# Kernel optimization log

Hardware: AMD Instinct MI355X
Metric: run time of the kernel (lower is better)

Reference implementation:

```python
import jax, jax.numpy as jnp
import numpy as np

B, NP, NR = 4, 2048, 10
EDGE_F = 32
EMB = 64          # emb_features == out_features (required for layer stacking)
ESM_EMB = 64
HEADS = 16
NUM_LAYERS = 4
LN_EPS = 1e-5


def _ln(x, g, b):
    mu = jnp.mean(x, axis=-1, keepdims=True)
    var = jnp.var(x, axis=-1, keepdims=True)
    return (x - mu) / jnp.sqrt(var + LN_EPS) * g + b


def setup_inputs() -> dict:
    key = jax.random.key(0)
    ks = jax.random.split(key, 32)
    s = 0.05  # xavier-ish scale for weights
    inp = {
        "pep_feat": jax.random.normal(ks[0], (B, NP, 27 + 1280), jnp.float32),
        "rec_feat": jax.random.normal(ks[1], (B, NP, NR, 42 + 1280), jnp.float32),
        "edge_feat": jax.random.normal(ks[2], (B, NP, NR, EDGE_F), jnp.float32),
        # embedding weights (torch Linear convention: y = x @ W.T)
        "W_rec_esm": jax.random.normal(ks[3], (ESM_EMB, 1280), jnp.float32) * s,
        "W_pep_esm": jax.random.normal(ks[4], (ESM_EMB, 1280), jnp.float32) * s,
        "W_pep_emb": jax.random.normal(ks[5], (EMB, 27 + ESM_EMB), jnp.float32) * s,
        "W_rec_emb": jax.random.normal(ks[6], (EMB, 21 + ESM_EMB), jnp.float32) * s,
        "W_edge_emb": jax.random.normal(ks[7], (EMB, EDGE_F), jnp.float32) * s,
        "pep_ln_g": jnp.ones((EMB,), jnp.float32),
        "pep_ln_b": jnp.zeros((EMB,), jnp.float32),
        "rec_ln_g": jnp.ones((EMB,), jnp.float32),
        "rec_ln_b": jnp.zeros((EMB,), jnp.float32),
        # stacked GraphAttention layer params [L, ...]
        "ga_Wp": jax.random.normal(ks[8], (NUM_LAYERS, EMB, EMB), jnp.float32) * s,
        "ga_bp": jnp.zeros((NUM_LAYERS, EMB), jnp.float32),
        "ga_Wr": jax.random.normal(ks[9], (NUM_LAYERS, EMB, 2 * EMB), jnp.float32) * s,
        "ga_br": jnp.zeros((NUM_LAYERS, EMB), jnp.float32),
        "ga_Wv": jax.random.normal(ks[10], (NUM_LAYERS, EMB, 2 * EMB), jnp.float32) * s,
        "ga_bv": jnp.zeros((NUM_LAYERS, EMB), jnp.float32),
        # self-attention pooling: LN + MLP [64 -> 64 -> 32 -> 16 heads], no biases
        "pool_ln_g": jnp.ones((EMB,), jnp.float32),
        "pool_ln_b": jnp.zeros((EMB,), jnp.float32),
        "pool_W0": jax.random.normal(ks[11], (EMB, EMB), jnp.float32) * s,
        "pool_W1": jax.random.normal(ks[12], (EMB // 2, EMB), jnp.float32) * s,
        "pool_W2": jax.random.normal(ks[13], (HEADS, EMB // 2), jnp.float32) * s,
        # final projection
        "mlp_W": jax.random.normal(ks[14], (EMB // 2, EMB), jnp.float32) * s,
        "mlp_b": jnp.zeros((EMB // 2,), jnp.float32),
    }
    return inp


def _forward(pep_feat, rec_feat, edge_feat, W_rec_esm, W_pep_esm, W_pep_emb,
             W_rec_emb, W_edge_emb, pep_ln_g, pep_ln_b, rec_ln_g, rec_ln_b,
             ga_Wp, ga_bp, ga_Wr, ga_br, ga_Wv, ga_bv,
             pool_ln_g, pool_ln_b, pool_W0, pool_W1, pool_W2, mlp_W, mlp_b):
    # --- embeddings ---
    rec_esm = rec_feat[..., 42:] @ W_rec_esm.T                       # [B,NP,10,ESM]
    pep_esm = pep_feat[..., -1280:] @ W_pep_esm.T                    # [B,NP,ESM]
    rec = jnp.concatenate([rec_feat[..., :21], rec_esm], axis=-1) @ W_rec_emb.T
    pep = jnp.concatenate([pep_feat[..., :27], pep_esm], axis=-1) @ W_pep_emb.T
    edge = edge_feat @ W_edge_emb.T                                  # [B,NP,10,EMB]
    pep = _ln(pep, pep_ln_g, pep_ln_b)
    rec = _ln(rec, rec_ln_g, rec_ln_b)

    inv_sqrt_d = 1.0 / np.sqrt(EMB).astype(np.float32)
    rec_edge = jnp.concatenate([rec, edge], axis=-1)                 # [B,NP,10,2*EMB]
    # --- stacked GraphAttention layers (dropout = eval-mode identity) ---
    for l in range(NUM_LAYERS):
        q = pep @ ga_Wp[l].T + ga_bp[l]                              # [B,NP,EMB]
        key = rec_edge @ ga_Wr[l].T + ga_br[l]                       # [B,NP,10,EMB]
        val = rec_edge @ ga_Wv[l].T + ga_bv[l]                       # [B,NP,10,EMB]
        logit = jnp.einsum('bpd,bprd->bpr', q, key) * inv_sqrt_d     # [B,NP,10]
        attn = jax.nn.softmax(logit, axis=-1)
        pep = q + jnp.einsum('bpr,bprd->bpd', attn, val)             # [B,NP,EMB]

    # --- self-attention pooling (note: softmax applied twice, as in source) ---
    d = _ln(pep, pool_ln_g, pool_ln_b)                               # [B,NP,EMB]
    h = jnp.tanh(d @ pool_W0.T)
    h = jnp.tanh(h @ pool_W1.T)
    logits = h @ pool_W2.T                                           # [B,NP,HEADS]
    a = jax.nn.softmax(logits, axis=1)
    a = jax.nn.softmax(a, axis=1)
    attended = jnp.einsum('bsh,bsd->bhd', a, d)                      # [B,HEADS,EMB]
    pooled = attended.mean(axis=1)                                   # [B,EMB]
    return pooled @ mlp_W.T + mlp_b                                  # [B,EMB//2]


def reference(pep_feat, rec_feat, edge_feat, W_rec_esm, W_pep_esm, W_pep_emb,
              W_rec_emb, W_edge_emb, pep_ln_g, pep_ln_b, rec_ln_g, rec_ln_b,
              ga_Wp, ga_bp, ga_Wr, ga_br, ga_Wv, ga_bv,
              pool_ln_g, pool_ln_b, pool_W0, pool_W1, pool_W2, mlp_W, mlp_b):
    return _forward(pep_feat, rec_feat, edge_feat, W_rec_esm, W_pep_esm, W_pep_emb,
                    W_rec_emb, W_edge_emb, pep_ln_g, pep_ln_b, rec_ln_g, rec_ln_b,
                    ga_Wp, ga_bp, ga_Wr, ga_br, ga_Wv, ga_bv,
                    pool_ln_g, pool_ln_b, pool_W0, pool_W1, pool_W2, mlp_W, mlp_b)
```

## Files before the change

kernel.cpp:

```cpp
#include <hip/hip_runtime.h>
#include <hip/hip_bf16.h>


typedef __attribute__((ext_vector_type(8))) short bf16x8;
typedef __attribute__((ext_vector_type(4))) float f32x4;

#define MFMA(a, b, c) __builtin_amdgcn_mfma_f32_16x16x32_bf16((a), (b), (c), 0, 0, 0)

#define WB_REC_OFF   0
#define WB_PEP_OFF   83968
#define WB_EDGE_OFF  167936
#define WB_P_OFF     169984
#define WB_R_OFF     186368
#define WB_V_OFF     219136
#define WB_W0_OFF    251904
#define WB_W1_OFF    256000
#define WB_W2_OFF    258048
#define WB_TOTAL     258560

__device__ __forceinline__ unsigned short f2bf(float x) {
  __hip_bfloat16 h = __float2bfloat16(x);
  return __builtin_bit_cast(unsigned short, h);
}
__device__ __forceinline__ float bf2f(unsigned short u) {
  unsigned int t = ((unsigned int)u) << 16;
  return __builtin_bit_cast(float, t);
}
__device__ __forceinline__ bf16x8 loadBc(const unsigned short* base, int chunk, int lane) {
  return *(const bf16x8*)(base + ((size_t)chunk * 64 + lane) * 8);
}
__device__ __forceinline__ float tanhf_fast(float x) {
  float e = __expf(2.f * x);
  return 1.f - 2.f / (e + 1.f);
}
__device__ __forceinline__ int swzr(int r) {
  return (r & 1) | (((r >> 1) & 7) << 2);
}

__global__ __launch_bounds__(256) void k_pack(
    const float* __restrict__ Wresm, const float* __restrict__ Wpesm,
    const float* __restrict__ Wre, const float* __restrict__ Wpe,
    const float* __restrict__ Wedge, const float* __restrict__ Wp,
    const float* __restrict__ Wr, const float* __restrict__ Wv,
    const float* __restrict__ W0, const float* __restrict__ W1,
    const float* __restrict__ W2, unsigned short* __restrict__ WB) {
  const int t = blockIdx.x * 256 + threadIdx.x;
  if (t >= WB_TOTAL) return;
  float v = 0.f;
  if (t < WB_EDGE_OFF) {
    bool isPep = (t >= WB_PEP_OFF);
    int u = isPep ? (t - WB_PEP_OFF) : t;
    int j = u & 7, lane = (u >> 3) & 63, n = (u >> 9) & 3, kc = u >> 11;
    int k = kc * 32 + ((lane >> 4) << 3) + j;
    int col = n * 16 + (lane & 15);
    if (kc < 40) {
      const float* wemb = isPep ? (Wpe + col * 91 + 27) : (Wre + col * 85 + 21);
      const float* wesm = isPep ? Wpesm : Wresm;
      float s = 0.f;
#pragma unroll 8
      for (int e = 0; e < 64; ++e) s += wemb[e] * wesm[e * 1280 + k];
      v = s;
    } else {
      int kl = k - 1280;
      if (isPep) v = (kl < 27) ? Wpe[col * 91 + kl] : 0.f;
      else       v = (kl < 21) ? Wre[col * 85 + kl] : 0.f;
    }
  } else if (t < WB_P_OFF) {
    int u = t - WB_EDGE_OFF;
    int j = u & 7, lane = (u >> 3) & 63, n = (u >> 9) & 3;
    v = Wedge[(n * 16 + (lane & 15)) * 32 + ((lane >> 4) << 3) + j];
  } else if (t < WB_R_OFF) {
    int u = t - WB_P_OFF;
    int l = u >> 12, w = u & 4095;
    int j = w & 7, lane = (w >> 3) & 63, n = (w >> 9) & 3, kc = w >> 11;
    int o = kc * 32 + ((lane >> 4) << 3) + j;
    int d = n * 16 + (lane & 15);
    v = Wp[l * 4096 + d * 64 + o];
  } else if (t < WB_V_OFF) {
    int u = t - WB_R_OFF;
    int l = u >> 13, w = u & 8191;
    int j = w & 7, lane = (w >> 3) & 63, c = (w >> 9) & 15;
    int kc = c >> 3, n = c & 7;
    int o = kc * 32 + ((lane >> 4) << 3) + j;
    int k = n * 16 + (lane & 15);
    v = Wr[l * 8192 + o * 128 + k];
  } else if (t < WB_W0_OFF) {
    int u = t - WB_V_OFF;
    int l = u >> 13, w = u & 8191;
    int j = w & 7, lane = (w >> 3) & 63, n = (w >> 9) & 3, kc = w >> 11;
    int k = kc * 32 + ((lane >> 4) << 3) + j;
    int d = n * 16 + (lane & 15);
    v = Wv[l * 8192 + d * 128 + k];
  } else if (t < WB_W1_OFF) {
    int u = t - WB_W0_OFF;
    int j = u & 7, lane = (u >> 3) & 63, c = u >> 9;
    int kc = c >> 2, n = c & 3;
    v = W0[(n * 16 + (lane & 15)) * 64 + kc * 32 + ((lane >> 4) << 3) + j];
  } else if (t < WB_W2_OFF) {
    int u = t - WB_W1_OFF;
    int j = u & 7, lane = (u >> 3) & 63, c = u >> 9;
    int kc = c >> 1, n = c & 1;
    v = W1[(n * 16 + (lane & 15)) * 64 + kc * 32 + ((lane >> 4) << 3) + j];
  } else {
    int u = t - WB_W2_OFF;
    int j = u & 7, lane = (u >> 3) & 63;
    v = W2[(lane & 15) * 32 + ((lane >> 4) << 3) + j];
  }
  WB[t] = f2bf(v);
}

__global__ __launch_bounds__(64) void k_emb(
    const float* __restrict__ rec_feat, const float* __restrict__ edge_feat,
    const float* __restrict__ pep_feat, const unsigned short* __restrict__ WB,
    const float* __restrict__ rec_g, const float* __restrict__ rec_b,
    const float* __restrict__ pep_g, const float* __restrict__ pep_b,
    unsigned short* __restrict__ rec_edge, unsigned short* __restrict__ pep_out) {
  __shared__ float stg[2][16][128];
  const int bid = blockIdx.x;
  const int lane = threadIdx.x;
  const int quad = lane >> 4, lr = lane & 15;
  const bool isPep = (bid >= 5120);
  const int brow = (isPep ? bid - 5120 : bid) * 16;

  const f32x4 fz = {0.f, 0.f, 0.f, 0.f};
  f32x4 acc[4] = {fz, fz, fz, fz};

  auto frag = [&](int buf, int c) -> bf16x8 {
    const int u0 = c * 8 + quad * 2;
    const int s0 = u0 ^ swzr(lr), s1 = (u0 + 1) ^ swzr(lr);
    const float4 f0 = *(const float4*)((const char*)&stg[buf][lr][0] + s0 * 16);
    const float4 f1 = *(const float4*)((const char*)&stg[buf][lr][0] + s1 * 16);
    bf16x8 a;
#pragma unroll
    for (int j = 0; j < 4; ++j) { a[j] = (short)f2bf(f0[j]); a[4 + j] = (short)f2bf(f1[j]); }
    return a;
  };

  if (!isPep) {
    const float* base = rec_feat + (size_t)brow * 1322 + 42;
    float2 ld2[16];
    auto loadg = [&](int g) {
#pragma unroll
      for (int i = 0; i < 16; ++i)
        ld2[i] = *(const float2*)(base + (size_t)i * 1322 + g * 128 + lane * 2);
    };
    auto writeg = [&](int b) {
#pragma unroll
      for (int i = 0; i < 16; ++i) {
        const int su = (lane >> 1) ^ swzr(i);
        *(float2*)((char*)&stg[b][i][0] + su * 16 + (lane & 1) * 8) = ld2[i];
      }
    };
    loadg(0); writeg(0);
    int buf = 0;
    for (int g = 0; g < 10; ++g) {
      bf16x8 bb[16];
#pragma unroll
      for (int m = 0; m < 16; ++m) bb[m] = loadBc(WB + WB_REC_OFF, g * 16 + m, lane);
      if (g < 9) loadg(g + 1);
#pragma unroll
      for (int c = 0; c < 4; ++c) {
        const bf16x8 a = frag(buf, c);
#pragma unroll
        for (int n = 0; n < 4; ++n) acc[n] = MFMA(a, bb[c * 4 + n], acc[n]);
      }
      if (g < 9) writeg(buf ^ 1);
      buf ^= 1;
    }
    {
      const float* p = rec_feat + (size_t)(brow + lr) * 1322 + quad * 8;
      bf16x8 a;
#pragma unroll
      for (int m = 0; m < 4; ++m) {
        const float2 v = *(const float2*)(p + 2 * m);
        a[2 * m] = (short)f2bf(v.x); a[2 * m + 1] = (short)f2bf(v.y);
      }
#pragma unroll
      for (int n = 0; n < 4; ++n)
        acc[n] = MFMA(a, loadBc(WB + WB_REC_OFF, 160 + n, lane), acc[n]);
    }
  } else {
    const float* base = pep_feat + (size_t)brow * 1307 + 27;
    float ldp[32];
    auto loadg = [&](int g) {
#pragma unroll
      for (int i = 0; i < 16; ++i)
#pragma unroll
        for (int ph = 0; ph < 2; ++ph)
          ldp[i * 2 + ph] = base[(size_t)i * 1307 + g * 128 + ph * 64 + lane];
    };
    auto writeg = [&](int b) {
#pragma unroll
      for (int i = 0; i < 16; ++i)
#pragma unroll
        for (int ph = 0; ph < 2; ++ph) {
          const int su = (ph * 16 + (lane >> 2)) ^ swzr(i);
          *((float*)((char*)&stg[b][i][0] + su * 16 + (lane & 3) * 4)) = ldp[i * 2 + ph];
        }
    };
    loadg(0); writeg(0);
    int buf = 0;
    for (int g = 0; g < 10; ++g) {
      bf16x8 bb[16];
#pragma unroll
      for (int m = 0; m < 16; ++m) bb[m] = loadBc(WB + WB_PEP_OFF, g * 16 + m, lane);
      if (g < 9) loadg(g + 1);
#pragma unroll
      for (int c = 0; c < 4; ++c) {
        const bf16x8 a = frag(buf, c);
#pragma unroll
        for (int n = 0; n < 4; ++n) acc[n] = MFMA(a, bb[c * 4 + n], acc[n]);
      }
      if (g < 9) writeg(buf ^ 1);
      buf ^= 1;
    }
    {
      const float* p = pep_feat + (size_t)(brow + lr) * 1307 + quad * 8;
      bf16x8 a;
#pragma unroll
      for (int j = 0; j < 8; ++j) a[j] = (short)f2bf(p[j]);
#pragma unroll
      for (int n = 0; n < 4; ++n)
        acc[n] = MFMA(a, loadBc(WB + WB_PEP_OFF, 160 + n, lane), acc[n]);
    }
  }

  float s[4], sq[4];
#pragma unroll
  for (int i = 0; i < 4; ++i) {
    s[i] = acc[0][i] + acc[1][i] + acc[2][i] + acc[3][i];
    sq[i] = acc[0][i] * acc[0][i] + acc[1][i] * acc[1][i] +
            acc[2][i] * acc[2][i] + acc[3][i] * acc[3][i];
  }
#pragma unroll
  for (int msk = 1; msk < 16; msk <<= 1) {
#pragma unroll
    for (int i = 0; i < 4; ++i) {
      s[i] += __shfl_xor(s[i], msk);
      sq[i] += __shfl_xor(sq[i], msk);
    }
  }
  const float* gp = isPep ? pep_g : rec_g;
  const float* bp = isPep ? pep_b : rec_b;
  float gv[4], bvl[4];
#pragma unroll
  for (int n = 0; n < 4; ++n) { gv[n] = gp[lr + 16 * n]; bvl[n] = bp[lr + 16 * n]; }

  if (!isPep) {
    f32x4 acce[4] = {fz, fz, fz, fz};
    {
      const float* p = edge_feat + (size_t)(brow + lr) * 32 + quad * 8;
      const float4 f0 = *(const float4*)(p);
      const float4 f1 = *(const float4*)(p + 4);
      bf16x8 a;
#pragma unroll
      for (int j = 0; j < 4; ++j) { a[j] = (short)f2bf(f0[j]); a[4 + j] = (short)f2bf(f1[j]); }
#pragma unroll
      for (int n = 0; n < 4; ++n) acce[n] = MFMA(a, loadBc(WB + WB_EDGE_OFF, n, lane), acce[n]);
    }
#pragma unroll
    for (int i = 0; i < 4; ++i) {
      const float mean = s[i] * (1.f / 64.f);
      const float var = sq[i] * (1.f / 64.f) - mean * mean;
      const float rstd = rsqrtf(var + 1e-5f);
      unsigned short* dst = rec_edge + (size_t)(brow + quad * 4 + i) * 128;
#pragma unroll
      for (int n = 0; n < 4; ++n) {
        dst[lr + 16 * n] = f2bf((acc[n][i] - mean) * rstd * gv[n] + bvl[n]);
        dst[64 + lr + 16 * n] = f2bf(acce[n][i]);
      }
    }
  } else {
#pragma unroll
    for (int i = 0; i < 4; ++i) {
      const float mean = s[i] * (1.f / 64.f);
      const float var = sq[i] * (1.f / 64.f) - mean * mean;
      const float rstd = rsqrtf(var + 1e-5f);
      unsigned short* dst = pep_out + (size_t)(brow + quad * 4 + i) * 64;
#pragma unroll
      for (int n = 0; n < 4; ++n)
        dst[lr + 16 * n] = f2bf((acc[n][i] - mean) * rstd * gv[n] + bvl[n]);
    }
  }
}

__global__ __launch_bounds__(256) void k_ga(
    const unsigned short* __restrict__ rec_edge, const unsigned short* __restrict__ pep_bf,
    const unsigned short* __restrict__ WB,
    const float* __restrict__ ga_bp, const float* __restrict__ ga_bv,
    const float* __restrict__ pool_g, const float* __restrict__ pool_b,
    float* __restrict__ dbuf, float* __restrict__ logitsT) {
  __shared__ unsigned short pep_s[1024];
  __shared__ unsigned short q_s[1024];
  __shared__ __align__(16) unsigned short zs[2048];
  __shared__ float bias_s[512];
  __shared__ float lgp[4][10][17];
  __shared__ float redp[4][2][16];
  __shared__ float oap[4][16][68];

  const int tid = threadIdx.x;
  const int w = tid >> 6;
  const int lane = tid & 63;
  const int quad = lane >> 4, lr = lane & 15;
  const int swz = lr & 7;
  const int pbase = blockIdx.x * 16;
  const int mycol = lr + 16 * w;
  const f32x4 fz = {0.f, 0.f, 0.f, 0.f};

  bias_s[tid] = ga_bp[tid & 255];
  bias_s[256 + tid] = ga_bv[tid & 255];
  if (tid < 128) {
    const int p = tid >> 3, gg = tid & 7;
    const bf16x8 v = *(const bf16x8*)(pep_bf + (size_t)(pbase + p) * 64 + gg * 8);
    *(bf16x8*)(pep_s + p * 64 + ((gg ^ (p & 7)) << 3)) = v;
  }
  const unsigned short* reb =
      rec_edge + (size_t)(pbase + lr) * 1280 + w * 32 + quad * 8;
  bf16x8 rfs[10];
#pragma unroll
  for (int r = 0; r < 10; ++r) rfs[r] = *(const bf16x8*)(reb + r * 128);
  __syncthreads();

  auto bwrite = [&](unsigned short* buf, int p, int col, unsigned short val) {
    buf[p * 64 + ((((col >> 3)) ^ (p & 7)) << 3) + (col & 7)] = val;
  };
  auto bfrag = [&](const unsigned short* buf, int kc) -> bf16x8 {
    return *(const bf16x8*)(buf + lr * 64 + ((((kc << 2) + quad) ^ swz) << 3));
  };

  f32x4 pcur;
  for (int l = 0; l < 4; ++l) {
    const unsigned short* WBp = WB + WB_P_OFF + l * 4096;
    const unsigned short* WBr = WB + WB_R_OFF + l * 8192;
    const unsigned short* WBv = WB + WB_V_OFF + l * 8192;

    f32x4 qa = fz;
    qa = MFMA(bfrag(pep_s, 0), loadBc(WBp, w, lane), qa);
    qa = MFMA(bfrag(pep_s, 1), loadBc(WBp, 4 + w, lane), qa);
    const float bpv = bias_s[l * 64 + mycol];
#pragma unroll
    for (int i = 0; i < 4; ++i) qa[i] += bpv;
#pragma unroll
    for (int i = 0; i < 4; ++i) bwrite(q_s, quad * 4 + i, mycol, f2bf(qa[i]));
    __syncthreads();

    const bf16x8 aq0 = bfrag(q_s, 0), aq1 = bfrag(q_s, 1);
    f32x4 za0 = fz, za1 = fz;
    za0 = MFMA(aq0, loadBc(WBr, 2 * w, lane), za0);
    za0 = MFMA(aq1, loadBc(WBr, 8 + 2 * w, lane), za0);
    za1 = MFMA(aq0, loadBc(WBr, 2 * w + 1, lane), za1);
    za1 = MFMA(aq1, loadBc(WBr, 9 + 2 * w, lane), za1);
#pragma unroll
    for (int i = 0; i < 4; ++i) {
      const int p = quad * 4 + i;
      const int k0 = 16 * (2 * w) + lr, k1 = 16 * (2 * w + 1) + lr;
      zs[p * 128 + ((((k0 >> 3) ^ (p & 7)) << 3) | (k0 & 7))] = f2bf(za0[i]);
      zs[p * 128 + ((((k1 >> 3) ^ (p & 7)) << 3) | (k1 & 7))] = f2bf(za1[i]);
    }
    float zfw[8];
    {
      const bf16x8 z8 = *(const bf16x8*)(zs + lr * 128 + (((quad + 4 * w) ^ swz) << 3));
#pragma unroll
      for (int j = 0; j < 8; ++j) zfw[j] = bf2f((unsigned short)z8[j]);
    }
#pragma unroll
    for (int r = 0; r < 10; ++r) {
      float part = 0.f;
#pragma unroll
      for (int j = 0; j < 8; ++j) part += bf2f((unsigned short)rfs[r][j]) * zfw[j];
      part += __shfl_xor(part, 16);
      part += __shfl_xor(part, 32);
      if (quad == 0) lgp[w][r][lr] = part;
    }
    __syncthreads();
    float lg[10];
#pragma unroll
    for (int r = 0; r < 10; ++r)
      lg[r] = (lgp[0][r][lr] + lgp[1][r][lr] + lgp[2][r][lr] + lgp[3][r][lr]) * 0.125f;
    float mx = lg[0];
#pragma unroll
    for (int r = 1; r < 10; ++r) mx = fmaxf(mx, lg[r]);
    float ssum = 0.f;
#pragma unroll
    for (int r = 0; r < 10; ++r) { lg[r] = __expf(lg[r] - mx); ssum += lg[r]; }
    const float inv = 1.f / ssum;
#pragma unroll
    for (int r = 0; r < 10; ++r) lg[r] *= inv;
    float wsacc[8] = {};
#pragma unroll
    for (int r = 0; r < 10; ++r)
#pragma unroll
      for (int j = 0; j < 8; ++j)
        wsacc[j] += lg[r] * bf2f((unsigned short)rfs[r][j]);
    bf16x8 wf;
#pragma unroll
    for (int j = 0; j < 8; ++j) wf[j] = (short)f2bf(wsacc[j]);
    f32x4 oa[4];
#pragma unroll
    for (int n = 0; n < 4; ++n) oa[n] = MFMA(wf, loadBc(WBv, w * 4 + n, lane), fz);
#pragma unroll
    for (int n = 0; n < 4; ++n)
#pragma unroll
      for (int i = 0; i < 4; ++i)
        oap[w][quad * 4 + i][n * 16 + lr] = oa[n][i];
    __syncthreads();
    const float bvv = bias_s[256 + l * 64 + mycol];
#pragma unroll
    for (int i = 0; i < 4; ++i) {
      const int p = quad * 4 + i;
      const float o = oap[0][p][mycol] + oap[1][p][mycol] +
                      oap[2][p][mycol] + oap[3][p][mycol];
      pcur[i] = qa[i] + o + bvv;
    }
#pragma unroll
    for (int i = 0; i < 4; ++i) bwrite(pep_s, quad * 4 + i, mycol, f2bf(pcur[i]));
    __syncthreads();
  }

  {
    float s[4], sq[4];
#pragma unroll
    for (int i = 0; i < 4; ++i) { s[i] = pcur[i]; sq[i] = pcur[i] * pcur[i]; }
#pragma unroll
    for (int msk = 1; msk < 16; msk <<= 1) {
#pragma unroll
      for (int i = 0; i < 4; ++i) {
        s[i] += __shfl_xor(s[i], msk);
        sq[i] += __shfl_xor(sq[i], msk);
      }
    }
    if (lr == 0) {
#pragma unroll
      for (int i = 0; i < 4; ++i) {
        redp[w][0][quad * 4 + i] = s[i];
        redp[w][1][quad * 4 + i] = sq[i];
      }
    }
    __syncthreads();
    const float gv = pool_g[mycol], bv2 = pool_b[mycol];
    float d[4];
    float* zf32 = (float*)zs;
#pragma unroll
    for (int i = 0; i < 4; ++i) {
      const int p = quad * 4 + i;
      const float sf = redp[0][0][p] + redp[1][0][p] + redp[2][0][p] + redp[3][0][p];
      const float sqf = redp[0][1][p] + redp[1][1][p] + redp[2][1][p] + redp[3][1][p];
      const float mean = sf * (1.f / 64.f);
      const float var = sqf * (1.f / 64.f) - mean * mean;
      const float rstd = rsqrtf(var + 1e-5f);
      d[i] = (pcur[i] - mean) * rstd * gv + bv2;
      zf32[p * 64 + mycol] = d[i];
      bwrite(q_s, p, mycol, f2bf(d[i]));
    }
    __syncthreads();
    {
      const float4 v = *(const float4*)(&zf32[tid * 4]);
      *(float4*)(dbuf + (size_t)pbase * 64 + tid * 4) = v;
    }
    if (w == 0) {
      const bf16x8 ad0 = bfrag(q_s, 0), ad1 = bfrag(q_s, 1);
      f32x4 h0[4] = {fz, fz, fz, fz};
#pragma unroll
      for (int n = 0; n < 4; ++n) {
        h0[n] = MFMA(ad0, loadBc(WB + WB_W0_OFF, n, lane), h0[n]);
        h0[n] = MFMA(ad1, loadBc(WB + WB_W0_OFF, 4 + n, lane), h0[n]);
      }
#pragma unroll
      for (int n = 0; n < 4; ++n)
#pragma unroll
        for (int i = 0; i < 4; ++i)
          bwrite(q_s, quad * 4 + i, lr + 16 * n, f2bf(tanhf_fast(h0[n][i])));
      const bf16x8 ah00 = bfrag(q_s, 0), ah01 = bfrag(q_s, 1);
      f32x4 h1[2] = {fz, fz};
#pragma unroll
      for (int n = 0; n < 2; ++n) {
        h1[n] = MFMA(ah00, loadBc(WB + WB_W1_OFF, n, lane), h1[n]);
        h1[n] = MFMA(ah01, loadBc(WB + WB_W1_OFF, 2 + n, lane), h1[n]);
      }
#pragma unroll
      for (int n = 0; n < 2; ++n)
#pragma unroll
        for (int i = 0; i < 4; ++i)
          bwrite(q_s, quad * 4 + i, lr + 16 * n, f2bf(tanhf_fast(h1[n][i])));
      const bf16x8 ah1 = bfrag(q_s, 0);
      f32x4 lac = MFMA(ah1, loadBc(WB + WB_W2_OFF, 0, lane), fz);
      const int b = pbase >> 11, sx0 = pbase & 2047;
#pragma unroll
      for (int i = 0; i < 4; ++i)
        logitsT[(size_t)(b * 16 + lr) * 2048 + sx0 + quad * 4 + i] = lac[i];
    }
  }
}

__global__ __launch_bounds__(256) void k_pool2(
    const float* __restrict__ logitsT, const float* __restrict__ dbuf,
    float* __restrict__ attp) {
  __shared__ float sh[2048];
  __shared__ float red[8];
  __shared__ float part[16][64];
  const int blk = blockIdx.x;
  const int bh = blk >> 2, q = blk & 3;
  const int b = bh >> 4;
  const int tid = threadIdx.x, lane = tid & 63, wid = tid >> 6;
  const float* lrow = logitsT + (size_t)bh * 2048;

  float m = -1e30f;
  for (int sx = tid; sx < 2048; sx += 256) {
    float v = lrow[sx];
    sh[sx] = v;
    m = fmaxf(m, v);
  }
#pragma unroll
  for (int msk = 1; msk < 64; msk <<= 1) m = fmaxf(m, __shfl_xor(m, msk));
  if (lane == 0) red[wid] = m;
  __syncthreads();
  m = fmaxf(fmaxf(red[0], red[1]), fmaxf(red[2], red[3]));

  float s1 = 0.f;
  for (int sx = tid; sx < 2048; sx += 256) {
    float e = __expf(sh[sx] - m);
    sh[sx] = e;
    s1 += e;
  }
#pragma unroll
  for (int msk = 1; msk < 64; msk <<= 1) s1 += __shfl_xor(s1, msk);
  __syncthreads();
  if (lane == 0) red[4 + wid] = s1;
  __syncthreads();
  s1 = red[4] + red[5] + red[6] + red[7];
  const float invS1 = 1.f / s1;

  float s2 = 0.f;
  for (int sx = tid; sx < 2048; sx += 256) {
    float e2 = __expf((sh[sx] - 1.f) * invS1);
    sh[sx] = e2;
    s2 += e2;
  }
#pragma unroll
  for (int msk = 1; msk < 64; msk <<= 1) s2 += __shfl_xor(s2, msk);
  __syncthreads();
  if (lane == 0) red[wid] = s2;
  __syncthreads();
  s2 = red[0] + red[1] + red[2] + red[3];
  const float invS2 = 1.f / s2;

  const int d16 = tid & 15, sxg = tid >> 4;
  float4 a4 = {0.f, 0.f, 0.f, 0.f};
  const float* db = dbuf + (size_t)b * 2048 * 64 + d16 * 4;
#pragma unroll 4
  for (int sx = q * 512 + sxg; sx < (q + 1) * 512; sx += 16) {
    const float w = sh[sx];
    const float4 v = *(const float4*)(db + (size_t)sx * 64);
    a4.x += w * v.x; a4.y += w * v.y; a4.z += w * v.z; a4.w += w * v.w;
  }
  *(float4*)(&part[sxg][d16 * 4]) = a4;
  __syncthreads();
  if (tid < 64) {
    float s = 0.f;
#pragma unroll
    for (int g2 = 0; g2 < 16; ++g2) s += part[g2][tid];
    attp[(size_t)(bh * 4 + q) * 64 + tid] = s * invS2;
  }
}

__global__ __launch_bounds__(256) void k_final(
    const float* __restrict__ attp, const float* __restrict__ W,
    const float* __restrict__ bias, float* __restrict__ out) {
  __shared__ float pooled[4][64];
  const int tid = threadIdx.x;
  {
    const int b = tid >> 6, d = tid & 63;
    float s = 0.f;
#pragma unroll
    for (int hq = 0; hq < 64; ++hq) s += attp[((size_t)b * 64 + hq) * 64 + d];
    pooled[b][d] = s * (1.f / 16.f);
  }
  __syncthreads();
  if (tid < 128) {
    const int b = tid >> 5, j = tid & 31;
    float s = bias[j];
#pragma unroll
    for (int d2 = 0; d2 < 64; ++d2) s += pooled[b][d2] * W[j * 64 + d2];
    out[b * 32 + j] = s;
  }
}

extern "C" void kernel_launch(void* const* d_in, const int* in_sizes, int n_in,
                              void* d_out, int out_size, void* d_ws, size_t ws_size,
                              hipStream_t stream) {
  const float* pep_feat = (const float*)d_in[0];
  const float* rec_feat = (const float*)d_in[1];
  const float* edge_feat = (const float*)d_in[2];
  const float* W_rec_esm = (const float*)d_in[3];
  const float* W_pep_esm = (const float*)d_in[4];
  const float* W_pep_emb = (const float*)d_in[5];
  const float* W_rec_emb = (const float*)d_in[6];
  const float* W_edge_emb = (const float*)d_in[7];
  const float* pep_ln_g = (const float*)d_in[8];
  const float* pep_ln_b = (const float*)d_in[9];
  const float* rec_ln_g = (const float*)d_in[10];
  const float* rec_ln_b = (const float*)d_in[11];
  const float* ga_Wp = (const float*)d_in[12];
  const float* ga_bp = (const float*)d_in[13];
  const float* ga_Wr = (const float*)d_in[14];
  const float* ga_br = (const float*)d_in[15];
  const float* ga_Wv = (const float*)d_in[16];
  const float* ga_bv = (const float*)d_in[17];
  const float* pool_ln_g = (const float*)d_in[18];
  const float* pool_ln_b = (const float*)d_in[19];
  const float* pool_W0 = (const float*)d_in[20];
  const float* pool_W1 = (const float*)d_in[21];
  const float* pool_W2 = (const float*)d_in[22];
  const float* mlp_W = (const float*)d_in[23];
  const float* mlp_b = (const float*)d_in[24];
  float* out = (float*)d_out;
  (void)ga_br;
  (void)ws_size; (void)in_sizes; (void)n_in; (void)out_size;

  char* ws = (char*)d_ws;
  unsigned short* WB = (unsigned short*)(ws);
  unsigned short* rec_edge = (unsigned short*)(ws + 524288);
  unsigned short* pep_bf = (unsigned short*)(ws + 21495808);
  float* dbuf = (float*)(ws + 22544384);
  float* logitsT = (float*)(ws + 24641536);
  float* attp = (float*)(ws + 25165824);

  k_pack<<<1010, 256, 0, stream>>>(W_rec_esm, W_pep_esm, W_rec_emb, W_pep_emb,
                                   W_edge_emb, ga_Wp, ga_Wr, ga_Wv,
                                   pool_W0, pool_W1, pool_W2, WB);
  k_emb<<<5632, 64, 0, stream>>>(rec_feat, edge_feat, pep_feat, WB,
                                 rec_ln_g, rec_ln_b, pep_ln_g, pep_ln_b,
                                 rec_edge, pep_bf);
  k_ga<<<512, 256, 0, stream>>>(rec_edge, pep_bf, WB, ga_bp, ga_bv,
                                pool_ln_g, pool_ln_b, dbuf, logitsT);
  k_pool2<<<256, 256, 0, stream>>>(logitsT, dbuf, attp);
  k_final<<<1, 256, 0, stream>>>(attp, mlp_W, mlp_b, out);
}
```

Measured before the change: 170.3 us.

## Process two row tiles per embedding block with aligned vector loads and shifted weight packing

The embedding kernel now handles 32 rows per block instead of 16, so each loaded B fragment feeds two MFMA tiles and weight traffic per row is halved. The feature columns are re-based to 16-byte-aligned offsets (40 for rec, 24 for pep), so rows can be read with dwordx4/dwordx2 inline-asm loads. To keep the maths unchanged, the packed weights are shifted and the boundary columns are moved into the tail chunk. Explicit vmcnt waits replace compiler-tracked dependencies. This raises register and LDS use per block, halves the grid, and adds fragile index remapping.

Measured after the change: 181.9 us. +6.8%, slower.

```diff
diff --git a/kernel.cpp b/kernel.cpp
--- a/kernel.cpp
+++ b/kernel.cpp
@@ -4,6 +4,7 @@
 
 typedef __attribute__((ext_vector_type(8))) short bf16x8;
 typedef __attribute__((ext_vector_type(4))) float f32x4;
+typedef __attribute__((ext_vector_type(2))) float f32x2;
 
 #define MFMA(a, b, c) __builtin_amdgcn_mfma_f32_16x16x32_bf16((a), (b), (c), 0, 0, 0)
 
@@ -53,17 +54,31 @@
     int j = u & 7, lane = (u >> 3) & 63, n = (u >> 9) & 3, kc = u >> 11;
     int k = kc * 32 + ((lane >> 4) << 3) + j;
     int col = n * 16 + (lane & 15);
-    if (kc < 40) {
-      const float* wemb = isPep ? (Wpe + col * 91 + 27) : (Wre + col * 85 + 21);
-      const float* wesm = isPep ? Wpesm : Wresm;
+    const float* wemb = isPep ? (Wpe + col * 91 + 27) : (Wre + col * 85 + 21);
+    const float* wesm = isPep ? Wpesm : Wresm;
+    auto comb = [&](int e_idx) {
       float s = 0.f;
 #pragma unroll 8
-      for (int e = 0; e < 64; ++e) s += wemb[e] * wesm[e * 1280 + k];
-      v = s;
+      for (int e = 0; e < 64; ++e) s += wemb[e] * wesm[e * 1280 + e_idx];
+      return s;
+    };
+    if (kc < 40) {
+      if (!isPep) {
+        v = (k >= 2) ? comb(k - 2) : 0.f;
+      } else {
+        v = (k < 3) ? Wpe[col * 91 + 24 + k] : comb(k - 3);
+      }
     } else {
       int kl = k - 1280;
-      if (isPep) v = (kl < 27) ? Wpe[col * 91 + kl] : 0.f;
-      else       v = (kl < 21) ? Wre[col * 85 + kl] : 0.f;
+      if (!isPep) {
+        if (kl <= 20) v = Wre[col * 85 + kl];
+        else if (kl <= 22) v = comb(1278 + (kl - 21));
+        else v = 0.f;
+      } else {
+        if (kl <= 23) v = Wpe[col * 91 + kl];
+        else if (kl <= 26) v = comb(1277 + (kl - 24));
+        else v = 0.f;
+      }
     }
   } else if (t < WB_P_OFF) {
     int u = t - WB_EDGE_OFF;
@@ -115,21 +130,26 @@
     const float* __restrict__ rec_g, const float* __restrict__ rec_b,
     const float* __restrict__ pep_g, const float* __restrict__ pep_b,
     unsigned short* __restrict__ rec_edge, unsigned short* __restrict__ pep_out) {
-  __shared__ float stg[2][16][128];
+  __shared__ float stg[2][2][16][128];
   const int bid = blockIdx.x;
   const int lane = threadIdx.x;
   const int quad = lane >> 4, lr = lane & 15;
-  const bool isPep = (bid >= 5120);
-  const int brow = (isPep ? bid - 5120 : bid) * 16;
+  const bool isPep = (bid >= 2560);
+  const int brow = (isPep ? bid - 2560 : bid) * 32;
+  const unsigned short* WBb = WB + (isPep ? WB_PEP_OFF : WB_REC_OFF);
 
   const f32x4 fz = {0.f, 0.f, 0.f, 0.f};
-  f32x4 acc[4] = {fz, fz, fz, fz};
-
-  auto frag = [&](int buf, int c) -> bf16x8 {
+  f32x4 acc[2][4];
+#pragma unroll
+  for (int tt = 0; tt < 2; ++tt)
+#pragma unroll
+    for (int n = 0; n < 4; ++n) acc[tt][n] = fz;
+
+  auto frag = [&](int b, int tt, int c) -> bf16x8 {
     const int u0 = c * 8 + quad * 2;
     const int s0 = u0 ^ swzr(lr), s1 = (u0 + 1) ^ swzr(lr);
-    const float4 f0 = *(const float4*)((const char*)&stg[buf][lr][0] + s0 * 16);
-    const float4 f1 = *(const float4*)((const char*)&stg[buf][lr][0] + s1 * 16);
+    const float4 f0 = *(const float4*)((const char*)&stg[b][tt][lr][0] + s0 * 16);
+    const float4 f1 = *(const float4*)((const char*)&stg[b][tt][lr][0] + s1 * 16);
     bf16x8 a;
 #pragma unroll
     for (int j = 0; j < 4; ++j) { a[j] = (short)f2bf(f0[j]); a[4 + j] = (short)f2bf(f1[j]); }
@@ -137,149 +157,183 @@
   };
 
   if (!isPep) {
-    const float* base = rec_feat + (size_t)brow * 1322 + 42;
-    float2 ld2[16];
+    f32x4 a4[16];
     auto loadg = [&](int g) {
 #pragma unroll
-      for (int i = 0; i < 16; ++i)
-        ld2[i] = *(const float2*)(base + (size_t)i * 1322 + g * 128 + lane * 2);
+      for (int ii = 0; ii < 16; ++ii) {
+        const int rr = 2 * ii + (lane >> 5);
+        const float* p = rec_feat + (size_t)(brow + rr) * 1322 + 40 + g * 128 + (lane & 31) * 4;
+        asm volatile("global_load_dwordx4 %0, %1, off" : "=v"(a4[ii]) : "v"(p));
+      }
     };
     auto writeg = [&](int b) {
 #pragma unroll
-      for (int i = 0; i < 16; ++i) {
-        const int su = (lane >> 1) ^ swzr(i);
-        *(float2*)((char*)&stg[b][i][0] + su * 16 + (lane & 1) * 8) = ld2[i];
+      for (int ii = 0; ii < 16; ++ii) {
+        const int rr = 2 * ii + (lane >> 5);
+        const int tt = rr >> 4, ri = rr & 15;
+        const int su = (lane & 31) ^ swzr(ri);
+        *(f32x4*)((char*)&stg[b][tt][ri][0] + su * 16) = a4[ii];
       }
     };
-    loadg(0); writeg(0);
+    loadg(0);
+    asm volatile("s_waitcnt vmcnt(0)" ::: "memory");
+    writeg(0);
     int buf = 0;
     for (int g = 0; g < 10; ++g) {
-      bf16x8 bb[16];
-#pragma unroll
-      for (int m = 0; m < 16; ++m) bb[m] = loadBc(WB + WB_REC_OFF, g * 16 + m, lane);
       if (g < 9) loadg(g + 1);
 #pragma unroll
       for (int c = 0; c < 4; ++c) {
-        const bf16x8 a = frag(buf, c);
-#pragma unroll
-        for (int n = 0; n < 4; ++n) acc[n] = MFMA(a, bb[c * 4 + n], acc[n]);
-      }
-      if (g < 9) writeg(buf ^ 1);
+        bf16x8 bb[4];
+#pragma unroll
+        for (int n = 0; n < 4; ++n) bb[n] = loadBc(WBb, g * 16 + c * 4 + n, lane);
+        const bf16x8 a0 = frag(buf, 0, c), a1 = frag(buf, 1, c);
+#pragma unroll
+        for (int n = 0; n < 4; ++n) {
+          acc[0][n] = MFMA(a0, bb[n], acc[0][n]);
+          acc[1][n] = MFMA(a1, bb[n], acc[1][n]);
+        }
+      }
+      if (g < 9) {
+        asm volatile("s_waitcnt vmcnt(0)" ::: "memory");
+        writeg(buf ^ 1);
+      }
       buf ^= 1;
     }
-    {
-      const float* p = rec_feat + (size_t)(brow + lr) * 1322 + quad * 8;
+#pragma unroll
+    for (int tt = 0; tt < 2; ++tt) {
+      const float* row = rec_feat + (size_t)(brow + 16 * tt + lr) * 1322;
       bf16x8 a;
 #pragma unroll
-      for (int m = 0; m < 4; ++m) {
-        const float2 v = *(const float2*)(p + 2 * m);
-        a[2 * m] = (short)f2bf(v.x); a[2 * m + 1] = (short)f2bf(v.y);
+      for (int j = 0; j < 8; ++j) {
+        const int pos = quad * 8 + j;
+        float x = 0.f;
+        if (pos <= 20) x = row[pos];
+        else if (pos == 21) x = row[1320];
+        else if (pos == 22) x = row[1321];
+        a[j] = (short)f2bf(x);
       }
 #pragma unroll
       for (int n = 0; n < 4; ++n)
-        acc[n] = MFMA(a, loadBc(WB + WB_REC_OFF, 160 + n, lane), acc[n]);
+        acc[tt][n] = MFMA(a, loadBc(WBb, 160 + n, lane), acc[tt][n]);
     }
   } else {
-    const float* base = pep_feat + (size_t)brow * 1307 + 27;
-    float ldp[32];
+    f32x2 a2[32];
     auto loadg = [&](int g) {
 #pragma unroll
-      for (int i = 0; i < 16; ++i)
-#pragma unroll
-        for (int ph = 0; ph < 2; ++ph)
-          ldp[i * 2 + ph] = base[(size_t)i * 1307 + g * 128 + ph * 64 + lane];
+      for (int i = 0; i < 32; ++i) {
+        const float* p = pep_feat + (size_t)(brow + i) * 1307 + 24 + g * 128 + lane * 2;
+        asm volatile("global_load_dwordx2 %0, %1, off" : "=v"(a2[i]) : "v"(p));
+      }
     };
     auto writeg = [&](int b) {
 #pragma unroll
-      for (int i = 0; i < 16; ++i)
-#pragma unroll
-        for (int ph = 0; ph < 2; ++ph) {
-          const int su = (ph * 16 + (lane >> 2)) ^ swzr(i);
-          *((float*)((char*)&stg[b][i][0] + su * 16 + (lane & 3) * 4)) = ldp[i * 2 + ph];
-        }
+      for (int i = 0; i < 32; ++i) {
+        const int tt = i >> 4, ri = i & 15;
+        const int su = (lane >> 1) ^ swzr(ri);
+        *(f32x2*)((char*)&stg[b][tt][ri][0] + su * 16 + (lane & 1) * 8) = a2[i];
+      }
     };
-    loadg(0); writeg(0);
+    loadg(0);
+    asm volatile("s_waitcnt vmcnt(0)" ::: "memory");
+    writeg(0);
     int buf = 0;
     for (int g = 0; g < 10; ++g) {
-      bf16x8 bb[16];
-#pragma unroll
-      for (int m = 0; m < 16; ++m) bb[m] = loadBc(WB + WB_PEP_OFF, g * 16 + m, lane);
       if (g < 9) loadg(g + 1);
 #pragma unroll
       for (int c = 0; c < 4; ++c) {
-        const bf16x8 a = frag(buf, c);
-#pragma unroll
-        for (int n = 0; n < 4; ++n) acc[n] = MFMA(a, bb[c * 4 + n], acc[n]);
-      }
-      if (g < 9) writeg(buf ^ 1);
+        bf16x8 bb[4];
+#pragma unroll
+        for (int n = 0; n < 4; ++n) bb[n] = loadBc(WBb, g * 16 + c * 4 + n, lane);
+        const bf16x8 a0 = frag(buf, 0, c), a1 = frag(buf, 1, c);
+#pragma unroll
+        for (int n = 0; n < 4; ++n) {
+          acc[0][n] = MFMA(a0, bb[n], acc[0][n]);
+          acc[1][n] = MFMA(a1, bb[n], acc[1][n]);
+        }
+      }
+      if (g < 9) {
+        asm volatile("s_waitcnt vmcnt(0)" ::: "memory");
+        writeg(buf ^ 1);
+      }
       buf ^= 1;
     }
-    {
-      const float* p = pep_feat + (size_t)(brow + lr) * 1307 + quad * 8;
+#pragma unroll
+    for (int tt = 0; tt < 2; ++tt) {
+      const float* row = pep_feat + (size_t)(brow + 16 * tt + lr) * 1307;
       bf16x8 a;
 #pragma unroll
-      for (int j = 0; j < 8; ++j) a[j] = (short)f2bf(p[j]);
+      for (int j = 0; j < 8; ++j) {
+        const int pos = quad * 8 + j;
+        float x = 0.f;
+        if (pos <= 23) x = row[pos];
+        else if (pos <= 26) x = row[1304 + (pos - 24)];
+        a[j] = (short)f2bf(x);
+      }
 #pragma unroll
       for (int n = 0; n < 4; ++n)
-        acc[n] = MFMA(a, loadBc(WB + WB_PEP_OFF, 160 + n, lane), acc[n]);
-    }
-  }
-
-  float s[4], sq[4];
-#pragma unroll
-  for (int i = 0; i < 4; ++i) {
-    s[i] = acc[0][i] + acc[1][i] + acc[2][i] + acc[3][i];
-    sq[i] = acc[0][i] * acc[0][i] + acc[1][i] * acc[1][i] +
-            acc[2][i] * acc[2][i] + acc[3][i] * acc[3][i];
-  }
-#pragma unroll
-  for (int msk = 1; msk < 16; msk <<= 1) {
-#pragma unroll
-    for (int i = 0; i < 4; ++i) {
-      s[i] += __shfl_xor(s[i], msk);
-      sq[i] += __shfl_xor(sq[i], msk);
-    }
-  }
+        acc[tt][n] = MFMA(a, loadBc(WBb, 160 + n, lane), acc[tt][n]);
+    }
+  }
+
   const float* gp = isPep ? pep_g : rec_g;
   const float* bp = isPep ? pep_b : rec_b;
   float gv[4], bvl[4];
 #pragma unroll
   for (int n = 0; n < 4; ++n) { gv[n] = gp[lr + 16 * n]; bvl[n] = bp[lr + 16 * n]; }
 
-  if (!isPep) {
-    f32x4 acce[4] = {fz, fz, fz, fz};
-    {
-      const float* p = edge_feat + (size_t)(brow + lr) * 32 + quad * 8;
-      const float4 f0 = *(const float4*)(p);
-      const float4 f1 = *(const float4*)(p + 4);
-      bf16x8 a;
-#pragma unroll
-      for (int j = 0; j < 4; ++j) { a[j] = (short)f2bf(f0[j]); a[4 + j] = (short)f2bf(f1[j]); }
-#pragma unroll
-      for (int n = 0; n < 4; ++n) acce[n] = MFMA(a, loadBc(WB + WB_EDGE_OFF, n, lane), acce[n]);
-    }
+#pragma unroll
+  for (int tt = 0; tt < 2; ++tt) {
+    float s[4], sq[4];
 #pragma unroll
     for (int i = 0; i < 4; ++i) {
-      const float mean = s[i] * (1.f / 64.f);
-      const float var = sq[i] * (1.f / 64.f) - mean * mean;
-      const float rstd = rsqrtf(var + 1e-5f);
-      unsigned short* dst = rec_edge + (size_t)(brow + quad * 4 + i) * 128;
-#pragma unroll
-      for (int n = 0; n < 4; ++n) {
-        dst[lr + 16 * n] = f2bf((acc[n][i] - mean) * rstd * gv[n] + bvl[n]);
-        dst[64 + lr + 16 * n] = f2bf(acce[n][i]);
-      }
-    }
-  } else {
-#pragma unroll
-    for (int i = 0; i < 4; ++i) {
-      const float mean = s[i] * (1.f / 64.f);
-      const float var = sq[i] * (1.f / 64.f) - mean * mean;
-      const float rstd = rsqrtf(var + 1e-5f);
-      unsigned short* dst = pep_out + (size_t)(brow + quad * 4 + i) * 64;
-#pragma unroll
-      for (int n = 0; n < 4; ++n)
-        dst[lr + 16 * n] = f2bf((acc[n][i] - mean) * rstd * gv[n] + bvl[n]);
+      s[i] = acc[tt][0][i] + acc[tt][1][i] + acc[tt][2][i] + acc[tt][3][i];
+      sq[i] = acc[tt][0][i] * acc[tt][0][i] + acc[tt][1][i] * acc[tt][1][i] +
+              acc[tt][2][i] * acc[tt][2][i] + acc[tt][3][i] * acc[tt][3][i];
+    }
+#pragma unroll
+    for (int msk = 1; msk < 16; msk <<= 1) {
+#pragma unroll
+      for (int i = 0; i < 4; ++i) {
+        s[i] += __shfl_xor(s[i], msk);
+        sq[i] += __shfl_xor(sq[i], msk);
+      }
+    }
+    if (!isPep) {
+      f32x4 acce[4] = {fz, fz, fz, fz};
+      {
+        const float* p = edge_feat + (size_t)(brow + 16 * tt + lr) * 32 + quad * 8;
+        const float4 f0 = *(const float4*)(p);
+        const float4 f1 = *(const float4*)(p + 4);
+        bf16x8 a;
+#pragma unroll
+        for (int j = 0; j < 4; ++j) { a[j] = (short)f2bf(f0[j]); a[4 + j] = (short)f2bf(f1[j]); }
+#pragma unroll
+        for (int n = 0; n < 4; ++n)
+          acce[n] = MFMA(a, loadBc(WB + WB_EDGE_OFF, n, lane), acce[n]);
+      }
+#pragma unroll
+      for (int i = 0; i < 4; ++i) {
+        const float mean = s[i] * (1.f / 64.f);
+        const float var = sq[i] * (1.f / 64.f) - mean * mean;
+        const float rstd = rsqrtf(var + 1e-5f);
+        unsigned short* dst = rec_edge + (size_t)(brow + 16 * tt + quad * 4 + i) * 128;
+#pragma unroll
+        for (int n = 0; n < 4; ++n) {
+          dst[lr + 16 * n] = f2bf((acc[tt][n][i] - mean) * rstd * gv[n] + bvl[n]);
+          dst[64 + lr + 16 * n] = f2bf(acce[n][i]);
+        }
+      }
+    } else {
+#pragma unroll
+      for (int i = 0; i < 4; ++i) {
+        const float mean = s[i] * (1.f / 64.f);
+        const float var = sq[i] * (1.f / 64.f) - mean * mean;
+        const float rstd = rsqrtf(var + 1e-5f);
+        unsigned short* dst = pep_out + (size_t)(brow + 16 * tt + quad * 4 + i) * 64;
+#pragma unroll
+        for (int n = 0; n < 4; ++n)
+          dst[lr + 16 * n] = f2bf((acc[tt][n][i] - mean) * rstd * gv[n] + bvl[n]);
+      }
     }
   }
 }
@@ -628,7 +682,7 @@
   k_pack<<<1010, 256, 0, stream>>>(W_rec_esm, W_pep_esm, W_rec_emb, W_pep_emb,
                                    W_edge_emb, ga_Wp, ga_Wr, ga_Wv,
                                    pool_W0, pool_W1, pool_W2, WB);
-  k_emb<<<5632, 64, 0, stream>>>(rec_feat, edge_feat, pep_feat, WB,
+  k_emb<<<2816, 64, 0, stream>>>(rec_feat, edge_feat, pep_feat, WB,
                                  rec_ln_g, rec_ln_b, pep_ln_g, pep_ln_b,
                                  rec_edge, pep_bf);
   k_ga<<<512, 256, 0, stream>>>(rec_edge, pep_bf, WB, ga_bp, ga_bv,
```
